# Kernel optimization log

Measured on AMD Instinct MI355X. Metric: run time of the kernel, lower is better.

Reference implementation:

```python
import jax, jax.numpy as jnp
import numpy as np

N_NODES = 50000
IN_CH = 128
HID = 128
OUT_CH = 40
N_LAYERS = 3
N_EDGES = 600000


def setup_inputs() -> dict:
    key = jax.random.key(0)
    ks = jax.random.split(key, 4 + 5 * N_LAYERS)
    x = jax.random.normal(ks[0], (N_NODES, IN_CH), dtype=jnp.float32)
    edge_attr = jax.random.normal(ks[1], (N_EDGES, 4), dtype=jnp.float32)
    edge_index = jax.random.randint(ks[2], (2, N_EDGES), 0, N_NODES, dtype=jnp.int64)
    # Per-layer MLP params ([in->hid->hid]); in==hid so stack as [L, d, d].
    def glorot(k, fan_in, fan_out):
        s = jnp.sqrt(2.0 / (fan_in + fan_out)).astype(jnp.float32)
        return jax.random.normal(k, (fan_in, fan_out), dtype=jnp.float32) * s
    W1 = jnp.stack([glorot(ks[3 + i], IN_CH if i == 0 else HID, HID) for i in range(N_LAYERS)])
    b1 = jnp.zeros((N_LAYERS, HID), dtype=jnp.float32)
    W2 = jnp.stack([glorot(ks[3 + N_LAYERS + i], HID, HID) for i in range(N_LAYERS)])
    b2 = jnp.zeros((N_LAYERS, HID), dtype=jnp.float32)
    Wc = glorot(ks[3 + 2 * N_LAYERS], HID, OUT_CH)
    bc = jnp.zeros((OUT_CH,), dtype=jnp.float32)
    return {"x": x, "edge_attr": edge_attr, "edge_index": edge_index,
            "W1": W1, "b1": b1, "W2": W2, "b2": b2, "Wc": Wc, "bc": bc}


def reference(x, edge_attr, edge_index, W1, b1, W2, b2, Wc, bc):
    # GIN node classifier, eval mode (dropout = identity, BN = identity).
    src, dst = edge_index[0], edge_index[1]
    h = x
    for i in range(N_LAYERS):
        # GINConv (eps=0): aggregate sum of neighbor features via scatter-add.
        msgs = h[src]                                   # [E, d] gather
        aggr = jax.ops.segment_sum(msgs, dst, num_segments=N_NODES)  # [N, d]
        z = h + aggr                                    # (1+eps)*x + sum
        z = jax.nn.relu(z @ W1[i] + b1[i])              # MLP hidden
        z = z @ W2[i] + b2[i]                           # MLP out
        h = jax.nn.relu(z)                              # F.relu(conv(...))
    return h @ Wc + bc                                  # [N, OUT_CH]
```

## Files before the change

### kernel.cpp

```cpp
#include <hip/hip_runtime.h>

#define N_NODES 50000
#define IN_CH 128
#define HID 128
#define OUT_CH 40
#define N_LAYERS 3
#define N_EDGES 600000
#define DSTRIDE 64
#define DEGSTRIDE 16

typedef __attribute__((ext_vector_type(8))) short short8;
typedef __attribute__((ext_vector_type(4))) float floatx4;

static __device__ __forceinline__ unsigned short f32_to_bf16(float f) {
  unsigned u = __float_as_uint(f);
  unsigned r = 0x7FFFu + ((u >> 16) & 1u);
  return (unsigned short)((u + r) >> 16);
}
static __device__ __forceinline__ float bf16_to_f32(unsigned short h) {
  return __uint_as_float(((unsigned)h) << 16);
}

#define ZERO_BLOCKS 782
__global__ __launch_bounds__(256) void zero_deg_kernel(int* __restrict__ deg) {
  int i = (blockIdx.x * 256 + threadIdx.x) * 4;
  if (i < N_NODES * DEGSTRIDE) *(int4*)(deg + i) = make_int4(0, 0, 0, 0);
}

#define CSRB 586
#define CONV_BLOCKS 6250
#define W_BLOCKS 408

__global__ __launch_bounds__(256) void prep_csr_kernel(
    const float* __restrict__ x, const float* __restrict__ W1,
    const float* __restrict__ W2, const float* __restrict__ Wc,
    const int* __restrict__ ei, unsigned short* __restrict__ xb,
    unsigned short* __restrict__ WT, unsigned short* __restrict__ WcT,
    unsigned short* __restrict__ hb1, int* __restrict__ deg,
    int* __restrict__ col) {
  const int b = blockIdx.x;
  const int t = threadIdx.x;
  if (b < CSRB) {
    int base = (b * 256 + t) * 4;
    if (base < N_EDGES) {
      int4 s4 = *(const int4*)(ei + base);
      int4 d4 = *(const int4*)(ei + N_EDGES + base);
      int p0 = atomicAdd(&deg[(size_t)d4.x * DEGSTRIDE], 1);
      int p1 = atomicAdd(&deg[(size_t)d4.y * DEGSTRIDE], 1);
      int p2 = atomicAdd(&deg[(size_t)d4.z * DEGSTRIDE], 1);
      int p3 = atomicAdd(&deg[(size_t)d4.w * DEGSTRIDE], 1);
      col[(size_t)d4.x * DSTRIDE + p0] = s4.x;
      col[(size_t)d4.y * DSTRIDE + p1] = s4.y;
      col[(size_t)d4.z * DSTRIDE + p2] = s4.z;
      col[(size_t)d4.w * DSTRIDE + p3] = s4.w;
    }
  } else if (b < CSRB + CONV_BLOCKS) {
    int i = ((b - CSRB) * 256 + t) * 4;
    if (i < N_NODES * 128) {
      float4 v = *(const float4*)(x + i);
      ushort4 o;
      o.x = f32_to_bf16(v.x); o.y = f32_to_bf16(v.y);
      o.z = f32_to_bf16(v.z); o.w = f32_to_bf16(v.w);
      *(ushort4*)(xb + i) = o;
    }
  } else if (b < CSRB + CONV_BLOCKS + W_BLOCKS) {
    int o = (b - CSRB - CONV_BLOCKS) * 256 + t;
    if (o < 6 * 16384) {
      int mat = o >> 14;
      int r = o & 16383;
      int n = r >> 7;
      int k = r & 127;
      const float* W = (mat < 3) ? (W1 + (size_t)mat * 16384)
                                 : (W2 + (size_t)(mat - 3) * 16384);
      WT[(size_t)mat * 16384 + (size_t)n * 128 + k] =
          f32_to_bf16(W[(size_t)k * 128 + n]);
    } else if (o < 6 * 16384 + 48 * 128) {
      int r = o - 6 * 16384;
      int n = r >> 7;
      int k = r & 127;
      float v = (n < OUT_CH) ? Wc[(size_t)k * OUT_CH + n] : 0.0f;
      WcT[(size_t)n * 128 + k] = f32_to_bf16(v);
    }
  } else {
    if (t < 128) xb[(size_t)N_NODES * 128 + t] = 0;
    else hb1[(size_t)N_NODES * 128 + (t - 128)] = 0;
  }
}

__global__ __launch_bounds__(256) void aggregate_kernel(
    const unsigned short* __restrict__ h, const int* __restrict__ deg,
    const int* __restrict__ col, unsigned short* __restrict__ z) {
  int n = __builtin_amdgcn_readfirstlane(blockIdx.x * 4 + (threadIdx.x >> 6));
  int q = threadIdx.x & 63;
  const size_t co = (size_t)q * 2;
  ushort2 sv = *(const ushort2*)(h + (size_t)n * 128 + co);
  float ax[8], ay[8];
#pragma unroll
  for (int k = 0; k < 8; ++k) { ax[k] = 0.f; ay[k] = 0.f; }
  ax[0] = bf16_to_f32(sv.x);
  ay[0] = bf16_to_f32(sv.y);
  int dg = __builtin_amdgcn_readfirstlane(deg[(size_t)n * DEGSTRIDE]);
  int cnt = (dg + 15) & ~15;
  const int* cp = col + (size_t)n * DSTRIDE;
  for (int i = 0; i < cnt; i += 16) {
    int ss[16];
#pragma unroll
    for (int k = 0; k < 16; ++k) {
      int sl = cp[i + k];
      ss[k] = __builtin_amdgcn_readfirstlane((i + k < dg) ? sl : N_NODES);
    }
    ushort2 vv[16];
#pragma unroll
    for (int k = 0; k < 16; ++k)
      vv[k] = *(const ushort2*)(h + (size_t)ss[k] * 128 + co);
#pragma unroll
    for (int k = 0; k < 16; ++k) {
      ax[k & 7] += bf16_to_f32(vv[k].x);
      ay[k & 7] += bf16_to_f32(vv[k].y);
    }
  }
  float s0 = (ax[0] + ax[1]) + (ax[2] + ax[3]) + (ax[4] + ax[5]) + (ax[6] + ax[7]);
  float s1 = (ay[0] + ay[1]) + (ay[2] + ay[3]) + (ay[4] + ay[5]) + (ay[6] + ay[7]);
  ushort2 o;
  o.x = f32_to_bf16(s0);
  o.y = f32_to_bf16(s1);
  *(ushort2*)(z + (size_t)n * 128 + co) = o;
}

template <bool LAST>
__global__ __launch_bounds__(256) void layer_pair_kernel(
    const unsigned short* __restrict__ A, const unsigned short* __restrict__ WT1,
    const float* __restrict__ b1, const unsigned short* __restrict__ WT2,
    const float* __restrict__ b2, unsigned short* __restrict__ Z,
    const unsigned short* __restrict__ WcT, const float* __restrict__ bc,
    float* __restrict__ out, int M) {
  __shared__ __align__(16) unsigned short Wl[128][136];
  __shared__ __align__(16) unsigned short T[64][136];
  const int tid = threadIdx.x;
  const int w = tid >> 6;
  const int lane = tid & 63;
  const int qg = lane >> 4;
  const int ln = lane & 15;
  const int row0 = blockIdx.x * 64;
  const int rbase = w * 16;
  const int r0 = row0 + rbase + ln;
  const short8 zero8 = {0, 0, 0, 0, 0, 0, 0, 0};

#pragma unroll
  for (int j = 0; j < 8; ++j) {
    int slot = tid + j * 256;
    int row = slot >> 4;
    int kb = slot & 15;
    *(short8*)&Wl[row][kb * 8] = *(const short8*)(WT1 + (size_t)row * 128 + kb * 8);
  }
  __syncthreads();

  floatx4 acc[8];
#pragma unroll
  for (int ct = 0; ct < 8; ++ct) acc[ct] = (floatx4){0.f, 0.f, 0.f, 0.f};
#pragma unroll
  for (int ks = 0; ks < 4; ++ks) {
    const int koff = ks * 32 + qg * 8;
    short8 a = (r0 < M) ? *(const short8*)(A + (size_t)r0 * 128 + koff) : zero8;
#pragma unroll
    for (int ct = 0; ct < 8; ++ct) {
      short8 b = *(const short8*)&Wl[ct * 16 + ln][koff];
      acc[ct] = __builtin_amdgcn_mfma_f32_16x16x32_bf16(a, b, acc[ct], 0, 0, 0);
    }
  }
#pragma unroll
  for (int ct = 0; ct < 8; ++ct) {
    float bv = b1[ct * 16 + ln];
#pragma unroll
    for (int r = 0; r < 4; ++r) {
      float v = fmaxf(acc[ct][r] + bv, 0.0f);
      T[rbase + qg * 4 + r][ct * 16 + ln] = f32_to_bf16(v);
    }
  }

  __syncthreads();
#pragma unroll
  for (int j = 0; j < 8; ++j) {
    int slot = tid + j * 256;
    int row = slot >> 4;
    int kb = slot & 15;
    *(short8*)&Wl[row][kb * 8] = *(const short8*)(WT2 + (size_t)row * 128 + kb * 8);
  }
  __syncthreads();

  floatx4 acc2[8];
#pragma unroll
  for (int ct = 0; ct < 8; ++ct) acc2[ct] = (floatx4){0.f, 0.f, 0.f, 0.f};
#pragma unroll
  for (int ks = 0; ks < 4; ++ks) {
    const int koff = ks * 32 + qg * 8;
    short8 a = *(const short8*)&T[rbase + ln][koff];
#pragma unroll
    for (int ct = 0; ct < 8; ++ct) {
      short8 b = *(const short8*)&Wl[ct * 16 + ln][koff];
      acc2[ct] = __builtin_amdgcn_mfma_f32_16x16x32_bf16(a, b, acc2[ct], 0, 0, 0);
    }
  }
#pragma unroll
  for (int ct = 0; ct < 8; ++ct) {
    float bv = b2[ct * 16 + ln];
#pragma unroll
    for (int r = 0; r < 4; ++r) {
      float v = fmaxf(acc2[ct][r] + bv, 0.0f);
      T[rbase + qg * 4 + r][ct * 16 + ln] = f32_to_bf16(v);
    }
  }

  if (LAST) {
    floatx4 acc3[3];
#pragma unroll
    for (int ct = 0; ct < 3; ++ct) acc3[ct] = (floatx4){0.f, 0.f, 0.f, 0.f};
#pragma unroll
    for (int ks = 0; ks < 4; ++ks) {
      const int koff = ks * 32 + qg * 8;
      short8 a = *(const short8*)&T[rbase + ln][koff];
#pragma unroll
      for (int ct = 0; ct < 3; ++ct) {
        short8 b = *(const short8*)(WcT + (size_t)(ct * 16 + ln) * 128 + koff);
        acc3[ct] = __builtin_amdgcn_mfma_f32_16x16x32_bf16(a, b, acc3[ct], 0, 0, 0);
      }
    }
#pragma unroll
    for (int ct = 0; ct < 3; ++ct) {
      int colg = ct * 16 + ln;
      if (colg < OUT_CH) {
        float bv = bc[colg];
#pragma unroll
        for (int r = 0; r < 4; ++r) {
          int row = row0 + rbase + qg * 4 + r;
          if (row < M) out[(size_t)row * OUT_CH + colg] = acc3[ct][r] + bv;
        }
      }
    }
  } else {
    __syncthreads();
#pragma unroll
    for (int j = 0; j < 4; ++j) {
      int slot = tid + j * 256;
      int row = slot >> 4;
      int kb = slot & 15;
      if (row0 + row < M) {
        short8 v = *(const short8*)&T[row][kb * 8];
        *(short8*)(Z + (size_t)(row0 + row) * 128 + kb * 8) = v;
      }
    }
  }
}

extern "C" void kernel_launch(void* const* d_in, const int* in_sizes, int n_in,
                              void* d_out, int out_size, void* d_ws,
                              size_t ws_size, hipStream_t stream) {
  const float* x = (const float*)d_in[0];
  const int* ei = (const int*)d_in[2];
  const float* W1 = (const float*)d_in[3];
  const float* b1 = (const float*)d_in[4];
  const float* W2 = (const float*)d_in[5];
  const float* b2 = (const float*)d_in[6];
  const float* Wc = (const float*)d_in[7];
  const float* bc = (const float*)d_in[8];
  float* out = (float*)d_out;

  const size_t NF = (size_t)(N_NODES + 1) * 128;
  unsigned short* hb0 = (unsigned short*)d_ws;
  unsigned short* hb1 = hb0 + NF;
  unsigned short* xbf = hb1 + NF;
  unsigned short* WT = xbf + NF;
  unsigned short* WcT = WT + 6 * 16384;
  int* deg = (int*)(WcT + 48 * 128);
  int* col = deg + (size_t)N_NODES * DEGSTRIDE;

  const dim3 blk(256);
  const int aggr_grid = N_NODES / 4;
  const int pair_grid = (N_NODES + 63) / 64;

  zero_deg_kernel<<<ZERO_BLOCKS, blk, 0, stream>>>(deg);

  prep_csr_kernel<<<CSRB + CONV_BLOCKS + W_BLOCKS + 1, blk, 0, stream>>>(
      x, W1, W2, Wc, ei, xbf, WT, WcT, hb1, deg, col);

  const unsigned short* h = xbf;
  for (int l = 0; l < N_LAYERS; ++l) {
    aggregate_kernel<<<aggr_grid, blk, 0, stream>>>(h, deg, col, hb0);
    if (l < N_LAYERS - 1) {
      layer_pair_kernel<false><<<pair_grid, blk, 0, stream>>>(
          hb0, WT + (size_t)l * 16384, b1 + (size_t)l * 128,
          WT + (size_t)(3 + l) * 16384, b2 + (size_t)l * 128, hb1,
          nullptr, nullptr, nullptr, N_NODES);
      h = hb1;
    } else {
      layer_pair_kernel<true><<<pair_grid, blk, 0, stream>>>(
          hb0, WT + (size_t)l * 16384, b1 + (size_t)l * 128,
          WT + (size_t)(3 + l) * 16384, b2 + (size_t)l * 128, nullptr,
          WcT, bc, out, N_NODES);
    }
  }
}
```

Measured before the change: 243.2 us.

## Partition CSR build and aggregation by XCD to localize node data in L2

The CSR-build blocks are reassigned so that each XCD (block index mod 8) handles only edges whose destination falls in its own contiguous node range, with every block looping over all edge chunks. The aggregate kernel is likewise remapped so that blocks on one XCD process one contiguous chunk of destination nodes. The aim is to keep deg/col atomics and writes within a single XCD's L2 and to improve locality. In exchange, every CSR block now reads the whole edge list (8x more edge loads), and the aggregate grid is padded with early-exit blocks.

```diff
diff --git a/kernel.cpp b/kernel.cpp
--- a/kernel.cpp
+++ b/kernel.cpp
@@ -8,6 +8,8 @@
 #define N_EDGES 600000
 #define DSTRIDE 64
 #define DEGSTRIDE 16
+#define NXCD 8
+#define CHUNK 6250
 
 typedef __attribute__((ext_vector_type(8))) short short8;
 typedef __attribute__((ext_vector_type(4))) float floatx4;
@@ -27,7 +29,8 @@
   if (i < N_NODES * DEGSTRIDE) *(int4*)(deg + i) = make_int4(0, 0, 0, 0);
 }
 
-#define CSRB 586
+#define CSRB 1024
+#define ECHUNKS 586
 #define CONV_BLOCKS 6250
 #define W_BLOCKS 408
 
@@ -41,18 +44,29 @@
   const int b = blockIdx.x;
   const int t = threadIdx.x;
   if (b < CSRB) {
-    int base = (b * 256 + t) * 4;
-    if (base < N_EDGES) {
+    const int lo = (b & 7) * CHUNK;
+    const int hi = lo + CHUNK;
+    for (int c = (b >> 3); c < ECHUNKS; c += (CSRB >> 3)) {
+      int base = (c * 256 + t) * 4;
+      if (base >= N_EDGES) continue;
       int4 s4 = *(const int4*)(ei + base);
       int4 d4 = *(const int4*)(ei + N_EDGES + base);
-      int p0 = atomicAdd(&deg[(size_t)d4.x * DEGSTRIDE], 1);
-      int p1 = atomicAdd(&deg[(size_t)d4.y * DEGSTRIDE], 1);
-      int p2 = atomicAdd(&deg[(size_t)d4.z * DEGSTRIDE], 1);
-      int p3 = atomicAdd(&deg[(size_t)d4.w * DEGSTRIDE], 1);
-      col[(size_t)d4.x * DSTRIDE + p0] = s4.x;
-      col[(size_t)d4.y * DSTRIDE + p1] = s4.y;
-      col[(size_t)d4.z * DSTRIDE + p2] = s4.z;
-      col[(size_t)d4.w * DSTRIDE + p3] = s4.w;
+      if (d4.x >= lo && d4.x < hi) {
+        int p = atomicAdd(&deg[(size_t)d4.x * DEGSTRIDE], 1);
+        col[(size_t)d4.x * DSTRIDE + p] = s4.x;
+      }
+      if (d4.y >= lo && d4.y < hi) {
+        int p = atomicAdd(&deg[(size_t)d4.y * DEGSTRIDE], 1);
+        col[(size_t)d4.y * DSTRIDE + p] = s4.y;
+      }
+      if (d4.z >= lo && d4.z < hi) {
+        int p = atomicAdd(&deg[(size_t)d4.z * DEGSTRIDE], 1);
+        col[(size_t)d4.z * DSTRIDE + p] = s4.z;
+      }
+      if (d4.w >= lo && d4.w < hi) {
+        int p = atomicAdd(&deg[(size_t)d4.w * DEGSTRIDE], 1);
+        col[(size_t)d4.w * DSTRIDE + p] = s4.w;
+      }
     }
   } else if (b < CSRB + CONV_BLOCKS) {
     int i = ((b - CSRB) * 256 + t) * 4;
@@ -87,10 +101,15 @@
   }
 }
 
+#define AGGR_GRID 12504
 __global__ __launch_bounds__(256) void aggregate_kernel(
     const unsigned short* __restrict__ h, const int* __restrict__ deg,
     const int* __restrict__ col, unsigned short* __restrict__ z) {
-  int n = __builtin_amdgcn_readfirstlane(blockIdx.x * 4 + (threadIdx.x >> 6));
+  const int xcd = blockIdx.x & 7;
+  const int idx = blockIdx.x >> 3;
+  int local = idx * 4 + (threadIdx.x >> 6);
+  if (local >= CHUNK) return;
+  int n = __builtin_amdgcn_readfirstlane(xcd * CHUNK + local);
   int q = threadIdx.x & 63;
   const size_t co = (size_t)q * 2;
   ushort2 sv = *(const ushort2*)(h + (size_t)n * 128 + co);
@@ -275,7 +294,6 @@
   int* col = deg + (size_t)N_NODES * DEGSTRIDE;
 
   const dim3 blk(256);
-  const int aggr_grid = N_NODES / 4;
   const int pair_grid = (N_NODES + 63) / 64;
 
   zero_deg_kernel<<<ZERO_BLOCKS, blk, 0, stream>>>(deg);
@@ -285,7 +303,7 @@
 
   const unsigned short* h = xbf;
   for (int l = 0; l < N_LAYERS; ++l) {
-    aggregate_kernel<<<aggr_grid, blk, 0, stream>>>(h, deg, col, hb0);
+    aggregate_kernel<<<AGGR_GRID, blk, 0, stream>>>(h, deg, col, hb0);
     if (l < N_LAYERS - 1) {
       layer_pair_kernel<false><<<pair_grid, blk, 0, stream>>>(
           hb0, WT + (size_t)l * 16384, b1 + (size_t)l * 128,
```

Measured after the change: 237.9 us. 2.2% less time.
